# Kernel tuning notes

Measured on AMD Instinct MI355X. Metric: run time of the kernel, lower is better.

## Reference

```python
import jax, jax.numpy as jnp
import numpy as np

B, S, L = 8, 2048, 8
H, NH = 768, 12
DH = H // NH
NUM_REL = 100
LN_EPS = 1e-5


def setup_inputs() -> dict:
    key = jax.random.key(0)
    ks = jax.random.split(key, 16)
    inp = {
        'text_embeddings': jax.random.normal(ks[0], (B, S, H), dtype=jnp.float32),
        # values in [-1, 64); -1 marks 'no leaf' and is masked out
        'graph_structure': jax.random.randint(ks[1], (B, S, L), -1, 64, dtype=jnp.int64),
        'relation_ids': jax.random.randint(ks[2], (B, S, L), 0, NUM_REL, dtype=jnp.int64),
        'rel_table': jax.random.normal(ks[3], (NUM_REL, H), dtype=jnp.float32),
        'Wq': jax.random.normal(ks[4], (H, H), dtype=jnp.float32) / np.sqrt(H),
        'bq': jnp.zeros((H,), dtype=jnp.float32),
        'Wk': jax.random.normal(ks[5], (H, H), dtype=jnp.float32) / np.sqrt(H),
        'bk': jnp.zeros((H,), dtype=jnp.float32),
        'Wv': jax.random.normal(ks[6], (H, H), dtype=jnp.float32) / np.sqrt(H),
        'bv': jnp.zeros((H,), dtype=jnp.float32),
        'Wo': jax.random.normal(ks[7], (H, H), dtype=jnp.float32) / np.sqrt(H),
        'bo': jnp.zeros((H,), dtype=jnp.float32),
        'gamma': jnp.ones((H,), dtype=jnp.float32),
        'beta': jnp.zeros((H,), dtype=jnp.float32),
    }
    return inp


def reference(text_embeddings, graph_structure, relation_ids, rel_table,
              Wq, bq, Wk, bk, Wv, bv, Wo, bo, gamma, beta):
    b, s, h = text_embeddings.shape
    l = relation_ids.shape[2]
    # embedding gather (clamp -1 -> 0, masked later)
    rel_emb = rel_table[jnp.clip(relation_ids, 0, None)]  # [B,S,L,H]
    # projections; query has length-1 per root token
    q = (text_embeddings @ Wq + bq).reshape(b, s, NH, DH)          # [B,S,N,D]
    k = (rel_emb @ Wk + bk).reshape(b, s, l, NH, DH)               # [B,S,L,N,D]
    v = (rel_emb @ Wv + bv).reshape(b, s, l, NH, DH)
    scores = jnp.einsum('bsnd,bslnd->bsnl', q, k) / np.sqrt(DH)    # [B,S,N,L]
    mask = (graph_structure != -1)[:, :, None, :]                  # [B,S,1,L]
    scores = jnp.where(mask, scores, jnp.float32(-10000.0))
    probs = jax.nn.softmax(scores, axis=-1)                        # [B,S,N,L]
    ctx = jnp.einsum('bsnl,bslnd->bsnd', probs, v).reshape(b, s, h)
    out = ctx @ Wo + bo
    x = text_embeddings + out
    mu = jnp.mean(x, axis=-1, keepdims=True)
    var = jnp.mean(jnp.square(x - mu), axis=-1, keepdims=True)
    return (x - mu) * jax.lax.rsqrt(var + LN_EPS) * gamma + beta
```

## Files before the change

kernel.cpp:

```cpp
#include <hip/hip_runtime.h>
#include <hip/hip_bf16.h>

#define H 768
#define NH 12
#define DH 64
#define LL 8
#define NTOK 16384
#define NREL 100
#define NRELP 128
#define PADW 72

typedef __attribute__((ext_vector_type(8))) short short8;
typedef __attribute__((ext_vector_type(4))) float f32x4;

__device__ __forceinline__ float bf2f(ushort u) {
  union { unsigned int i; float f; } v; v.i = ((unsigned int)u) << 16; return v.f;
}
__device__ __forceinline__ float bflo(unsigned int u) {
  union { unsigned int i; float f; } v; v.i = u << 16; return v.f;
}
__device__ __forceinline__ float bfhi(unsigned int u) {
  union { unsigned int i; float f; } v; v.i = u & 0xffff0000u; return v.f;
}
__device__ __forceinline__ ushort f2bf(float f) {
  union { float f; unsigned int i; } v; v.f = f;
  unsigned int x = v.i;
  return (ushort)((x + 0x7fffu + ((x >> 16) & 1u)) >> 16);
}
__device__ __forceinline__ unsigned int cvt_pk_bf16(float lo, float hi) {
  unsigned int r;
  asm("v_cvt_pk_bf16_f32 %0, %1, %2" : "=v"(r) : "v"(lo), "v"(hi));
  return r;
}

__global__ __launch_bounds__(256) void prep_kernel(
    const float* __restrict__ s0, ushort* __restrict__ d0,
    const float* __restrict__ s1, ushort* __restrict__ d1,
    const float* __restrict__ s2, ushort* __restrict__ d2,
    const float* __restrict__ s3, ushort* __restrict__ d3,
    const float* __restrict__ rel, ushort* __restrict__ RelB) {
  if (blockIdx.z == 4) {
    int b = blockIdx.y * 24 + blockIdx.x;
    if (b < 96) {
      int i = (b * 256 + threadIdx.x) * 4;
      int row = i / H;
      ushort4 o = {0, 0, 0, 0};
      if (row < NREL) {
        float4 v = *(const float4*)(rel + i);
        o.x = f2bf(v.x); o.y = f2bf(v.y); o.z = f2bf(v.z); o.w = f2bf(v.w);
      }
      *(ushort4*)(RelB + i) = o;
    }
    return;
  }
  const float* src; ushort* dst;
  switch (blockIdx.z) {
    case 0:  src = s0; dst = d0; break;
    case 1:  src = s1; dst = d1; break;
    case 2:  src = s2; dst = d2; break;
    default: src = s3; dst = d3; break;
  }
  __shared__ float tile[32][33];
  int bx = blockIdx.x * 32, by = blockIdx.y * 32;
  int tx = threadIdx.x & 31, ty = threadIdx.x >> 5;
  #pragma unroll
  for (int i = 0; i < 32; i += 8)
    tile[ty + i][tx] = src[(size_t)(by + ty + i) * H + bx + tx];
  __syncthreads();
  #pragma unroll
  for (int i = 0; i < 32; i += 8)
    dst[(size_t)(bx + ty + i) * H + by + tx] = f2bf(tile[tx][ty + i]);
}

__device__ __forceinline__ void gload_lds16(const void* g, void* l) {
  __builtin_amdgcn_global_load_lds(
      (const __attribute__((address_space(1))) unsigned int*)g,
      (__attribute__((address_space(3))) unsigned int*)l, 16, 0, 0);
}

#define BM 128
#define BN 256
#define BK 64
#define ATILE (BM * BK)
#define BTILE (BN * BK)

#define GEMM_COMPUTE()                                                         \
  _Pragma("unroll")                                                            \
  for (int kk = 0; kk < 2; ++kk) {                                             \
    const int sw = (((kk << 2) | lk) ^ (lr & 7)) * 8;                          \
    short8 af[4], bfr[8];                                                      \
    _Pragma("unroll")                                                          \
    for (int m = 0; m < 4; ++m)                                                \
      af[m] = *(const short8*)(As + (wr * 64 + m * 16 + lr) * BK + sw);        \
    _Pragma("unroll")                                                          \
    for (int n = 0; n < 8; ++n)                                                \
      bfr[n] = *(const short8*)(Bs + (wc * 128 + n * 16 + lr) * BK + sw);      \
    _Pragma("unroll")                                                          \
    for (int m = 0; m < 4; ++m)                                                \
      _Pragma("unroll")                                                        \
      for (int n = 0; n < 8; ++n)                                              \
        acc[m][n] = __builtin_amdgcn_mfma_f32_16x16x32_bf16(af[m], bfr[n],     \
                                                            acc[m][n], 0, 0, 0);\
  }

#define GEMM_EPILOGUE()                                                        \
  _Pragma("unroll")                                                            \
  for (int m = 0; m < 4; ++m) {                                                \
    _Pragma("unroll")                                                          \
    for (int n = 0; n < 8; ++n) {                                              \
      int col = col0 + wc * 128 + n * 16 + lr;                                 \
      float b = bias[col];                                                     \
      _Pragma("unroll")                                                        \
      for (int j = 0; j < 4; ++j) {                                            \
        int row = row0 + wr * 64 + m * 16 + lk * 4 + j;                        \
        C[(size_t)row * N + col] = f2bf(acc[m][n][j] + b);                     \
      }                                                                        \
    }                                                                          \
  }

__device__ __forceinline__ void gemm_body(
    ushort* As, ushort* Bs,
    const ushort* __restrict__ A,
    const ushort* __restrict__ Bt,
    const float* __restrict__ bias,
    ushort* __restrict__ C,
    int M, int N, int K, int bx, int by) {
  const int tid = threadIdx.x;
  const int row0 = by * BM;
  const int col0 = bx * BN;
  const int wave = tid >> 6;
  const int lane = tid & 63;
  const int wr = wave >> 1, wc = wave & 1;
  const int lr = lane & 15, lk = lane >> 4;
  f32x4 acc[4][8];
  #pragma unroll
  for (int m = 0; m < 4; ++m)
    #pragma unroll
    for (int n = 0; n < 8; ++n) acc[m][n] = (f32x4)(0.f);

  for (int k0 = 0; k0 < K; k0 += BK) {
    #pragma unroll
    for (int i = 0; i < 4; ++i) {
      int c = tid + i * 256; int r = c >> 3, s = c & 7; int gsx = s ^ (r & 7);
      gload_lds16(A + (size_t)(row0 + r) * K + k0 + gsx * 8, (char*)As + c * 16);
    }
    #pragma unroll
    for (int i = 0; i < 8; ++i) {
      int c = tid + i * 256; int r = c >> 3, s = c & 7; int gsx = s ^ (r & 7);
      gload_lds16(Bt + (size_t)(col0 + r) * K + k0 + gsx * 8, (char*)Bs + c * 16);
    }
    __syncthreads();
    GEMM_COMPUTE()
    __syncthreads();
  }
  GEMM_EPILOGUE()
}

__device__ __forceinline__ void gemm_body_a32(
    ushort* As, ushort* Bs,
    const float* __restrict__ A32,
    const ushort* __restrict__ Bt,
    const float* __restrict__ bias,
    ushort* __restrict__ C,
    int M, int N, int K, int bx, int by) {
  const int tid = threadIdx.x;
  const int row0 = by * BM;
  const int col0 = bx * BN;
  const int wave = tid >> 6;
  const int lane = tid & 63;
  const int wr = wave >> 1, wc = wave & 1;
  const int lr = lane & 15, lk = lane >> 4;
  f32x4 acc[4][8];
  #pragma unroll
  for (int m = 0; m < 4; ++m)
    #pragma unroll
    for (int n = 0; n < 8; ++n) acc[m][n] = (f32x4)(0.f);

  for (int k0 = 0; k0 < K; k0 += BK) {
    #pragma unroll
    for (int i = 0; i < 8; ++i) {
      int c = tid + i * 256; int r = c >> 3, s = c & 7; int gsx = s ^ (r & 7);
      gload_lds16(Bt + (size_t)(col0 + r) * K + k0 + gsx * 8, (char*)Bs + c * 16);
    }
    #pragma unroll
    for (int i = 0; i < 4; ++i) {
      int c = tid + i * 256; int r = c >> 3, s = c & 7; int gsx = s ^ (r & 7);
      const float* src = A32 + (size_t)(row0 + r) * K + k0 + gsx * 8;
      float4 f0 = *(const float4*)(src);
      float4 f1 = *(const float4*)(src + 4);
      uint4 w;
      w.x = cvt_pk_bf16(f0.x, f0.y);
      w.y = cvt_pk_bf16(f0.z, f0.w);
      w.z = cvt_pk_bf16(f1.x, f1.y);
      w.w = cvt_pk_bf16(f1.z, f1.w);
      *(uint4*)((char*)As + c * 16) = w;
    }
    __syncthreads();
    GEMM_COMPUTE()
    __syncthreads();
  }
  GEMM_EPILOGUE()
}

__global__ __launch_bounds__(256, 2) void gemm_q_kv_kernel(
    const float* __restrict__ X, const ushort* __restrict__ WqT,
    const float* __restrict__ bq, ushort* __restrict__ Qbf,
    const ushort* __restrict__ RelB,
    const ushort* __restrict__ WkT, const float* __restrict__ bk, ushort* __restrict__ Ktab,
    const ushort* __restrict__ WvT, const float* __restrict__ bv, ushort* __restrict__ Vtab) {
  __shared__ ushort As[ATILE];
  __shared__ ushort Bs[BTILE];
  int lin = blockIdx.x;
  if (lin < 6) {
    if (lin < 3)
      gemm_body(As, Bs, RelB, WkT, bk, Ktab, NRELP, H, H, lin, 0);
    else
      gemm_body(As, Bs, RelB, WvT, bv, Vtab, NRELP, H, H, lin - 3, 0);
    return;
  }
  int l2 = lin - 6;
  int wg = (l2 & 7) * 48 + (l2 >> 3);
  gemm_body_a32(As, Bs, X, WqT, bq, Qbf, NTOK, H, H, wg % 3, wg / 3);
}

__global__ __launch_bounds__(256, 2) void gemm_bt_kernel(
    const ushort* __restrict__ A, const ushort* __restrict__ Bt,
    const float* __restrict__ bias, ushort* __restrict__ C,
    int M, int N, int K) {
  __shared__ ushort As[ATILE];
  __shared__ ushort Bs[BTILE];
  int lin = blockIdx.y * gridDim.x + blockIdx.x;
  int q = (gridDim.x * gridDim.y) >> 3;
  int wg = (lin & 7) * q + (lin >> 3);
  gemm_body(As, Bs, A, Bt, bias, C, M, N, K, wg % gridDim.x, wg / gridDim.x);
}

__global__ __launch_bounds__(256) void attn3_kernel(
    const ushort* __restrict__ Q,
    const ushort* __restrict__ Ktab,
    const ushort* __restrict__ Vtab,
    const int* __restrict__ graph,
    const int* __restrict__ relid,
    ushort* __restrict__ Ctx) {
  __shared__ __align__(16) ushort Ks[NREL * PADW];
  __shared__ __align__(16) ushort Vs[NREL * PADW];
  const int tid = threadIdx.x;
  const int head = blockIdx.y;
  const int t = blockIdx.x * 256 + tid;

  #pragma unroll
  for (int i = 0; i < 4; ++i) {
    int c = tid + i * 256;
    if (c < NREL * 9) {
      int row = c / 9, slot = c - row * 9;
      int gsx = (slot < 8) ? slot * 8 : 0;
      const size_t src = (size_t)row * H + head * DH + gsx;
      gload_lds16(Ktab + src, (char*)Ks + (size_t)c * 16);
      gload_lds16(Vtab + src, (char*)Vs + (size_t)c * 16);
    }
  }

  const uint4* qp = (const uint4*)(Q + (size_t)t * H + head * DH);
  uint4 qw[8];
  #pragma unroll
  for (int j = 0; j < 8; ++j) qw[j] = qp[j];
  const int4* gp = (const int4*)(graph + (size_t)t * LL);
  const int4* rp = (const int4*)(relid + (size_t)t * LL);
  int4 ga = gp[0], gb = gp[1];
  int4 ra = rp[0], rb = rp[1];
  int gs[8] = {ga.x, ga.y, ga.z, ga.w, gb.x, gb.y, gb.z, gb.w};
  int rid[8] = {ra.x, ra.y, ra.z, ra.w, rb.x, rb.y, rb.z, rb.w};
  int koff[8];
  #pragma unroll
  for (int l = 0; l < 8; ++l) {
    int r = rid[l] < 0 ? 0 : rid[l];
    koff[l] = r * (PADW * 2);
  }

  __syncthreads();

  float s[8];
  #pragma unroll
  for (int l = 0; l < 8; ++l) s[l] = 0.f;
  #pragma unroll
  for (int j = 0; j < 8; ++j) {
    float qf[8];
    qf[0] = bflo(qw[j].x); qf[1] = bfhi(qw[j].x);
    qf[2] = bflo(qw[j].y); qf[3] = bfhi(qw[j].y);
    qf[4] = bflo(qw[j].z); qf[5] = bfhi(qw[j].z);
    qf[6] = bflo(qw[j].w); qf[7] = bfhi(qw[j].w);
    #pragma unroll
    for (int l = 0; l < 8; ++l) {
      uint4 kw = *(const uint4*)((const char*)Ks + koff[l] + j * 16);
      s[l] += qf[0] * bflo(kw.x) + qf[1] * bfhi(kw.x)
            + qf[2] * bflo(kw.y) + qf[3] * bfhi(kw.y)
            + qf[4] * bflo(kw.z) + qf[5] * bfhi(kw.z)
            + qf[6] * bflo(kw.w) + qf[7] * bfhi(kw.w);
    }
  }

  #pragma unroll
  for (int l = 0; l < 8; ++l)
    s[l] = (gs[l] != -1) ? s[l] * 0.125f : -10000.0f;
  float mx = s[0];
  #pragma unroll
  for (int l = 1; l < 8; ++l) mx = fmaxf(mx, s[l]);
  float p[8], den = 0.f;
  #pragma unroll
  for (int l = 0; l < 8; ++l) { p[l] = __expf(s[l] - mx); den += p[l]; }
  float inv = 1.f / den;
  #pragma unroll
  for (int l = 0; l < 8; ++l) p[l] *= inv;

  ushort* cp = Ctx + (size_t)t * H + head * DH;
  #pragma unroll
  for (int j = 0; j < 8; ++j) {
    float a[8];
    #pragma unroll
    for (int d = 0; d < 8; ++d) a[d] = 0.f;
    #pragma unroll
    for (int l = 0; l < 8; ++l) {
      uint4 vw = *(const uint4*)((const char*)Vs + koff[l] + j * 16);
      a[0] += p[l] * bflo(vw.x); a[1] += p[l] * bfhi(vw.x);
      a[2] += p[l] * bflo(vw.y); a[3] += p[l] * bfhi(vw.y);
      a[4] += p[l] * bflo(vw.z); a[5] += p[l] * bfhi(vw.z);
      a[6] += p[l] * bflo(vw.w); a[7] += p[l] * bfhi(vw.w);
    }
    short8 o;
    #pragma unroll
    for (int d = 0; d < 8; ++d) o[d] = (short)f2bf(a[d]);
    *(short8*)(cp + j * 8) = o;
  }
}

__global__ __launch_bounds__(192) void ln_kernel(
    const float* __restrict__ text, const ushort* __restrict__ op,
    const float* __restrict__ gamma, const float* __restrict__ beta,
    float* __restrict__ out) {
  int t = blockIdx.x;
  int c0 = threadIdx.x * 4;
  float4 tv = *(const float4*)(text + (size_t)t * H + c0);
  ushort4 ov = *(const ushort4*)(op + (size_t)t * H + c0);
  float x0 = tv.x + bf2f(ov.x), x1 = tv.y + bf2f(ov.y);
  float x2 = tv.z + bf2f(ov.z), x3 = tv.w + bf2f(ov.w);
  float s = x0 + x1 + x2 + x3;
  float s2 = x0 * x0 + x1 * x1 + x2 * x2 + x3 * x3;
  #pragma unroll
  for (int off = 32; off > 0; off >>= 1) {
    s  += __shfl_xor(s, off, 64);
    s2 += __shfl_xor(s2, off, 64);
  }
  __shared__ float red[2][3];
  int wave = threadIdx.x >> 6, lane = threadIdx.x & 63;
  if (lane == 0) { red[0][wave] = s; red[1][wave] = s2; }
  __syncthreads();
  s  = red[0][0] + red[0][1] + red[0][2];
  s2 = red[1][0] + red[1][1] + red[1][2];
  float mu = s * (1.f / H);
  float var = s2 * (1.f / H) - mu * mu;
  float rs = rsqrtf(var + 1e-5f);
  float4 g4 = *(const float4*)(gamma + c0);
  float4 b4 = *(const float4*)(beta + c0);
  float4 o4;
  o4.x = (x0 - mu) * rs * g4.x + b4.x;
  o4.y = (x1 - mu) * rs * g4.y + b4.y;
  o4.z = (x2 - mu) * rs * g4.z + b4.z;
  o4.w = (x3 - mu) * rs * g4.w + b4.w;
  *(float4*)(out + (size_t)t * H + c0) = o4;
}

extern "C" void kernel_launch(void* const* d_in, const int* in_sizes, int n_in,
                              void* d_out, int out_size, void* d_ws, size_t ws_size,
                              hipStream_t stream) {
  const float* text      = (const float*)d_in[0];
  const int*   graph     = (const int*)d_in[1];
  const int*   relid     = (const int*)d_in[2];
  const float* rel_table = (const float*)d_in[3];
  const float* Wq = (const float*)d_in[4];  const float* bq = (const float*)d_in[5];
  const float* Wk = (const float*)d_in[6];  const float* bk = (const float*)d_in[7];
  const float* Wv = (const float*)d_in[8];  const float* bv = (const float*)d_in[9];
  const float* Wo = (const float*)d_in[10]; const float* bo = (const float*)d_in[11];
  const float* gamma = (const float*)d_in[12];
  const float* beta  = (const float*)d_in[13];
  float* out = (float*)d_out;
  char* ws = (char*)d_ws;

  const size_t TOKH = (size_t)NTOK * H;
  size_t off = 0;
  ushort* Ctx  = (ushort*)(ws + off); off += TOKH * 2;
  ushort* Qbf  = (ushort*)(ws + off); off += TOKH * 2;
  ushort* WqT  = (ushort*)(ws + off); off += (size_t)H * H * 2;
  ushort* WoT  = (ushort*)(ws + off); off += (size_t)H * H * 2;
  ushort* WkT  = (ushort*)(ws + off); off += (size_t)H * H * 2;
  ushort* WvT  = (ushort*)(ws + off); off += (size_t)H * H * 2;
  ushort* RelB = (ushort*)(ws + off); off += (size_t)NRELP * H * 2;
  ushort* Ktab = (ushort*)(ws + off); off += (size_t)NRELP * H * 2;
  ushort* Vtab = (ushort*)(ws + off); off += (size_t)NRELP * H * 2;

  prep_kernel<<<dim3(24, 24, 5), 256, 0, stream>>>(
      Wq, WqT, Wo, WoT, Wk, WkT, Wv, WvT, rel_table, RelB);
  gemm_q_kv_kernel<<<6 + 384, 256, 0, stream>>>(
      text, WqT, bq, Qbf, RelB, WkT, bk, Ktab, WvT, bv, Vtab);
  dim3 ga(NTOK / 256, NH);
  attn3_kernel<<<ga, 256, 0, stream>>>(Qbf, Ktab, Vtab, graph, relid, Ctx);
  dim3 g1(H / BN, NTOK / BM);
  gemm_bt_kernel<<<g1, 256, 0, stream>>>(Ctx, WoT, bo, Qbf, NTOK, H, H);
  ln_kernel<<<NTOK, 192, 0, stream>>>(text, Qbf, gamma, beta, out);
}
```

Before: 101.8 us.

## Double-buffer GEMM LDS tiles with async global-to-LDS loads and 8 waves

Rewrites both GEMM bodies as a two-stage pipeline. The tile for step t+2 is staged into the alternate LDS buffer with global_load_lds while the current buffer is consumed, and the loop uses explicit vmcnt waits and barriers. Workgroups grow to 512 threads (8 waves, 4x4 MFMA tiles per wave). The fp32 activation A tile for the Q projection is now copied straight into LDS and converted to bf16 when fragments are read, which removes the register round-trip in the global load path. The goal is to hide global-load latency behind MFMA work, at the cost of much larger LDS use (up to 128KB per block), which lowers block occupancy.

Measured after the change: 118.5 us. 16.4% more time.

```diff
diff --git a/kernel.cpp b/kernel.cpp
--- a/kernel.cpp
+++ b/kernel.cpp
@@ -81,34 +81,32 @@
 #define BM 128
 #define BN 256
 #define BK 64
-#define ATILE (BM * BK)
-#define BTILE (BN * BK)
-
-#define GEMM_COMPUTE()                                                         \
-  _Pragma("unroll")                                                            \
-  for (int kk = 0; kk < 2; ++kk) {                                             \
-    const int sw = (((kk << 2) | lk) ^ (lr & 7)) * 8;                          \
-    short8 af[4], bfr[8];                                                      \
-    _Pragma("unroll")                                                          \
-    for (int m = 0; m < 4; ++m)                                                \
-      af[m] = *(const short8*)(As + (wr * 64 + m * 16 + lr) * BK + sw);        \
-    _Pragma("unroll")                                                          \
-    for (int n = 0; n < 8; ++n)                                                \
-      bfr[n] = *(const short8*)(Bs + (wc * 128 + n * 16 + lr) * BK + sw);      \
-    _Pragma("unroll")                                                          \
-    for (int m = 0; m < 4; ++m)                                                \
-      _Pragma("unroll")                                                        \
-      for (int n = 0; n < 8; ++n)                                              \
-        acc[m][n] = __builtin_amdgcn_mfma_f32_16x16x32_bf16(af[m], bfr[n],     \
-                                                            acc[m][n], 0, 0, 0);\
-  }
-
-#define GEMM_EPILOGUE()                                                        \
+
+#define SBAR()   __builtin_amdgcn_s_barrier()
+#define SCHED0() __builtin_amdgcn_sched_barrier(0)
+
+#define STG_A16(k0, cbuf)                                                      \
+  _Pragma("unroll") for (int i = 0; i < 2; ++i) {                              \
+    int c = tid + i * 512; int r = c >> 3, s = c & 7; int g = s ^ (r & 7);     \
+    gload_lds16(A + (size_t)(row0 + r) * K + (k0) + g * 8,                     \
+                Ab + (cbuf) * 16384 + c * 16); }
+#define STG_A32(k0, cbuf)                                                      \
+  _Pragma("unroll") for (int i = 0; i < 4; ++i) {                              \
+    int c = tid + i * 512; int r = c >> 4, s = c & 15; int g = s ^ (r & 15);   \
+    gload_lds16(A32 + (size_t)(row0 + r) * K + (k0) + g * 4,                   \
+                Ab + (cbuf) * 32768 + c * 16); }
+#define STG_B(k0, cbuf)                                                        \
+  _Pragma("unroll") for (int i = 0; i < 4; ++i) {                              \
+    int c = tid + i * 512; int r = c >> 3, s = c & 7; int g = s ^ (r & 7);     \
+    gload_lds16(Bt + (size_t)(col0 + r) * K + (k0) + g * 8,                    \
+                Bb + (cbuf) * 32768 + c * 16); }
+
+#define PIPE_EPILOGUE()                                                        \
   _Pragma("unroll")                                                            \
   for (int m = 0; m < 4; ++m) {                                                \
     _Pragma("unroll")                                                          \
-    for (int n = 0; n < 8; ++n) {                                              \
-      int col = col0 + wc * 128 + n * 16 + lr;                                 \
+    for (int n = 0; n < 4; ++n) {                                              \
+      int col = col0 + wc * 64 + n * 16 + lr;                                  \
       float b = bias[col];                                                     \
       _Pragma("unroll")                                                        \
       for (int j = 0; j < 4; ++j) {                                            \
@@ -118,121 +116,154 @@
     }                                                                          \
   }
 
-__device__ __forceinline__ void gemm_body(
-    ushort* As, ushort* Bs,
-    const ushort* __restrict__ A,
-    const ushort* __restrict__ Bt,
-    const float* __restrict__ bias,
-    ushort* __restrict__ C,
+__device__ __forceinline__ void gemm_pipe_bf16(
+    char* Ab, char* Bb,
+    const ushort* __restrict__ A, const ushort* __restrict__ Bt,
+    const float* __restrict__ bias, ushort* __restrict__ C,
     int M, int N, int K, int bx, int by) {
   const int tid = threadIdx.x;
-  const int row0 = by * BM;
-  const int col0 = bx * BN;
-  const int wave = tid >> 6;
-  const int lane = tid & 63;
-  const int wr = wave >> 1, wc = wave & 1;
+  const int row0 = by * BM, col0 = bx * BN;
+  const int wave = tid >> 6, lane = tid & 63;
+  const int wr = wave >> 2, wc = wave & 3;
   const int lr = lane & 15, lk = lane >> 4;
-  f32x4 acc[4][8];
+  f32x4 acc[4][4];
   #pragma unroll
   for (int m = 0; m < 4; ++m)
     #pragma unroll
-    for (int n = 0; n < 8; ++n) acc[m][n] = (f32x4)(0.f);
-
-  for (int k0 = 0; k0 < K; k0 += BK) {
-    #pragma unroll
-    for (int i = 0; i < 4; ++i) {
-      int c = tid + i * 256; int r = c >> 3, s = c & 7; int gsx = s ^ (r & 7);
-      gload_lds16(A + (size_t)(row0 + r) * K + k0 + gsx * 8, (char*)As + c * 16);
-    }
-    #pragma unroll
-    for (int i = 0; i < 8; ++i) {
-      int c = tid + i * 256; int r = c >> 3, s = c & 7; int gsx = s ^ (r & 7);
-      gload_lds16(Bt + (size_t)(col0 + r) * K + k0 + gsx * 8, (char*)Bs + c * 16);
-    }
-    __syncthreads();
-    GEMM_COMPUTE()
-    __syncthreads();
-  }
-  GEMM_EPILOGUE()
-}
-
-__device__ __forceinline__ void gemm_body_a32(
-    ushort* As, ushort* Bs,
-    const float* __restrict__ A32,
-    const ushort* __restrict__ Bt,
-    const float* __restrict__ bias,
-    ushort* __restrict__ C,
+    for (int n = 0; n < 4; ++n) acc[m][n] = (f32x4)(0.f);
+  const int nt = K / BK;
+
+  STG_A16(0, 0) STG_B(0, 0)
+  STG_A16(BK, 1) STG_B(BK, 1)
+  asm volatile("s_waitcnt vmcnt(6)" ::: "memory");
+  SCHED0(); SBAR();
+  int cb = 0;
+  for (int t = 0; t < nt; ++t) {
+    #pragma unroll
+    for (int kk = 0; kk < 2; ++kk) {
+      const int sw = (((kk << 2) | lk) ^ (lr & 7)) * 16;
+      short8 af[4], bfr[4];
+      #pragma unroll
+      for (int m = 0; m < 4; ++m)
+        af[m] = *(const short8*)(Ab + cb * 16384 + (wr * 64 + m * 16 + lr) * 128 + sw);
+      #pragma unroll
+      for (int n = 0; n < 4; ++n)
+        bfr[n] = *(const short8*)(Bb + cb * 32768 + (wc * 64 + n * 16 + lr) * 128 + sw);
+      #pragma unroll
+      for (int m = 0; m < 4; ++m)
+        #pragma unroll
+        for (int n = 0; n < 4; ++n)
+          acc[m][n] = __builtin_amdgcn_mfma_f32_16x16x32_bf16(af[m], bfr[n], acc[m][n], 0, 0, 0);
+    }
+    if (t == nt - 1) break;
+    SBAR(); SCHED0();
+    if (t + 2 < nt) {
+      STG_A16((t + 2) * BK, cb) STG_B((t + 2) * BK, cb)
+      asm volatile("s_waitcnt vmcnt(6)" ::: "memory");
+    } else {
+      asm volatile("s_waitcnt vmcnt(0)" ::: "memory");
+    }
+    SCHED0(); SBAR();
+    cb ^= 1;
+  }
+  PIPE_EPILOGUE()
+}
+
+__device__ __forceinline__ void gemm_pipe_a32(
+    char* Ab, char* Bb,
+    const float* __restrict__ A32, const ushort* __restrict__ Bt,
+    const float* __restrict__ bias, ushort* __restrict__ C,
     int M, int N, int K, int bx, int by) {
   const int tid = threadIdx.x;
-  const int row0 = by * BM;
-  const int col0 = bx * BN;
-  const int wave = tid >> 6;
-  const int lane = tid & 63;
-  const int wr = wave >> 1, wc = wave & 1;
+  const int row0 = by * BM, col0 = bx * BN;
+  const int wave = tid >> 6, lane = tid & 63;
+  const int wr = wave >> 2, wc = wave & 3;
   const int lr = lane & 15, lk = lane >> 4;
-  f32x4 acc[4][8];
+  f32x4 acc[4][4];
   #pragma unroll
   for (int m = 0; m < 4; ++m)
     #pragma unroll
-    for (int n = 0; n < 8; ++n) acc[m][n] = (f32x4)(0.f);
-
-  for (int k0 = 0; k0 < K; k0 += BK) {
-    #pragma unroll
-    for (int i = 0; i < 8; ++i) {
-      int c = tid + i * 256; int r = c >> 3, s = c & 7; int gsx = s ^ (r & 7);
-      gload_lds16(Bt + (size_t)(col0 + r) * K + k0 + gsx * 8, (char*)Bs + c * 16);
-    }
-    #pragma unroll
-    for (int i = 0; i < 4; ++i) {
-      int c = tid + i * 256; int r = c >> 3, s = c & 7; int gsx = s ^ (r & 7);
-      const float* src = A32 + (size_t)(row0 + r) * K + k0 + gsx * 8;
-      float4 f0 = *(const float4*)(src);
-      float4 f1 = *(const float4*)(src + 4);
-      uint4 w;
-      w.x = cvt_pk_bf16(f0.x, f0.y);
-      w.y = cvt_pk_bf16(f0.z, f0.w);
-      w.z = cvt_pk_bf16(f1.x, f1.y);
-      w.w = cvt_pk_bf16(f1.z, f1.w);
-      *(uint4*)((char*)As + c * 16) = w;
-    }
-    __syncthreads();
-    GEMM_COMPUTE()
-    __syncthreads();
-  }
-  GEMM_EPILOGUE()
-}
-
-__global__ __launch_bounds__(256, 2) void gemm_q_kv_kernel(
+    for (int n = 0; n < 4; ++n) acc[m][n] = (f32x4)(0.f);
+  const int nt = K / BK;
+
+  STG_A32(0, 0) STG_B(0, 0)
+  STG_A32(BK, 1) STG_B(BK, 1)
+  asm volatile("s_waitcnt vmcnt(8)" ::: "memory");
+  SCHED0(); SBAR();
+  int cb = 0;
+  for (int t = 0; t < nt; ++t) {
+    #pragma unroll
+    for (int kk = 0; kk < 2; ++kk) {
+      const int sw = (((kk << 2) | lk) ^ (lr & 7)) * 16;
+      short8 af[4], bfr[4];
+      #pragma unroll
+      for (int m = 0; m < 4; ++m) {
+        const int R = wr * 64 + m * 16 + lr;
+        const int c0 = (kk << 3) + (lk << 1);
+        const char* base = Ab + cb * 32768 + R * 256;
+        union { uint4 u; float4 f; } fa, fb;
+        fa.u = *(const uint4*)(base + ((c0 ^ lr) * 16));
+        fb.u = *(const uint4*)(base + (((c0 + 1) ^ lr) * 16));
+        union { uint4 u; short8 s8; } w;
+        w.u.x = cvt_pk_bf16(fa.f.x, fa.f.y);
+        w.u.y = cvt_pk_bf16(fa.f.z, fa.f.w);
+        w.u.z = cvt_pk_bf16(fb.f.x, fb.f.y);
+        w.u.w = cvt_pk_bf16(fb.f.z, fb.f.w);
+        af[m] = w.s8;
+      }
+      #pragma unroll
+      for (int n = 0; n < 4; ++n)
+        bfr[n] = *(const short8*)(Bb + cb * 32768 + (wc * 64 + n * 16 + lr) * 128 + sw);
+      #pragma unroll
+      for (int m = 0; m < 4; ++m)
+        #pragma unroll
+        for (int n = 0; n < 4; ++n)
+          acc[m][n] = __builtin_amdgcn_mfma_f32_16x16x32_bf16(af[m], bfr[n], acc[m][n], 0, 0, 0);
+    }
+    if (t == nt - 1) break;
+    SBAR(); SCHED0();
+    if (t + 2 < nt) {
+      STG_A32((t + 2) * BK, cb) STG_B((t + 2) * BK, cb)
+      asm volatile("s_waitcnt vmcnt(8)" ::: "memory");
+    } else {
+      asm volatile("s_waitcnt vmcnt(0)" ::: "memory");
+    }
+    SCHED0(); SBAR();
+    cb ^= 1;
+  }
+  PIPE_EPILOGUE()
+}
+
+__global__ __launch_bounds__(512, 2) void gemm_q_kv_kernel(
     const float* __restrict__ X, const ushort* __restrict__ WqT,
     const float* __restrict__ bq, ushort* __restrict__ Qbf,
     const ushort* __restrict__ RelB,
     const ushort* __restrict__ WkT, const float* __restrict__ bk, ushort* __restrict__ Ktab,
     const ushort* __restrict__ WvT, const float* __restrict__ bv, ushort* __restrict__ Vtab) {
-  __shared__ ushort As[ATILE];
-  __shared__ ushort Bs[BTILE];
+  __shared__ char lds[131072];
   int lin = blockIdx.x;
   if (lin < 6) {
     if (lin < 3)
-      gemm_body(As, Bs, RelB, WkT, bk, Ktab, NRELP, H, H, lin, 0);
+      gemm_pipe_bf16(lds, lds + 65536, RelB, WkT, bk, Ktab, NRELP, H, H, lin, 0);
     else
-      gemm_body(As, Bs, RelB, WvT, bv, Vtab, NRELP, H, H, lin - 3, 0);
+      gemm_pipe_bf16(lds, lds + 65536, RelB, WvT, bv, Vtab, NRELP, H, H, lin - 3, 0);
     return;
   }
   int l2 = lin - 6;
   int wg = (l2 & 7) * 48 + (l2 >> 3);
-  gemm_body_a32(As, Bs, X, WqT, bq, Qbf, NTOK, H, H, wg % 3, wg / 3);
-}
-
-__global__ __launch_bounds__(256, 2) void gemm_bt_kernel(
+  gemm_pipe_a32(lds, lds + 65536, X, WqT, bq, Qbf, NTOK, H, H, wg % 3, wg / 3);
+}
+
+__global__ __launch_bounds__(512, 2) void gemm_bt_kernel(
     const ushort* __restrict__ A, const ushort* __restrict__ Bt,
     const float* __restrict__ bias, ushort* __restrict__ C,
     int M, int N, int K) {
-  __shared__ ushort As[ATILE];
-  __shared__ ushort Bs[BTILE];
+  __shared__ char lds[98304];
   int lin = blockIdx.y * gridDim.x + blockIdx.x;
   int q = (gridDim.x * gridDim.y) >> 3;
   int wg = (lin & 7) * q + (lin >> 3);
-  gemm_body(As, Bs, A, Bt, bias, C, M, N, K, wg % gridDim.x, wg / gridDim.x);
+  gemm_pipe_bf16(lds, lds + 32768, A, Bt, bias, C, M, N, K,
+                 wg % gridDim.x, wg / gridDim.x);
 }
 
 __global__ __launch_bounds__(256) void attn3_kernel(
@@ -399,11 +430,11 @@
 
   prep_kernel<<<dim3(24, 24, 5), 256, 0, stream>>>(
       Wq, WqT, Wo, WoT, Wk, WkT, Wv, WvT, rel_table, RelB);
-  gemm_q_kv_kernel<<<6 + 384, 256, 0, stream>>>(
+  gemm_q_kv_kernel<<<6 + 384, 512, 0, stream>>>(
       text, WqT, bq, Qbf, RelB, WkT, bk, Ktab, WvT, bv, Vtab);
   dim3 ga(NTOK / 256, NH);
   attn3_kernel<<<ga, 256, 0, stream>>>(Qbf, Ktab, Vtab, graph, relid, Ctx);
   dim3 g1(H / BN, NTOK / BM);
-  gemm_bt_kernel<<<g1, 256, 0, stream>>>(Ctx, WoT, bo, Qbf, NTOK, H, H);
+  gemm_bt_kernel<<<g1, 512, 0, stream>>>(Ctx, WoT, bo, Qbf, NTOK, H, H);
   ln_kernel<<<NTOK, 192, 0, stream>>>(text, Qbf, gamma, beta, out);
 }
```

## Fuse Q projection, attention and output projection into one persistent mega kernel

Applied to the files above, without the earlier changes.

Replaces the separate Q GEMM, attention and output GEMM launches with a single kernel. Each 512-thread block handles 64 tokens: it stages the full X row-block in LDS as bf16, computes Q into LDS per 256-column chunk, runs attention for four heads straight from that LDS Q, then restages Ctx and runs the Wo GEMM. The K/V table GEMMs move to a small separate 12-block kernel. This removes the Q round trip through global memory and two launches. In exchange, only 256 blocks run at one block per CU, attention reads K/V from global/L2 instead of LDS, and half the threads sit idle during attention.

After: 197.4 us. 93.9% more time.

```diff
diff --git a/kernel.cpp b/kernel.cpp
--- a/kernel.cpp
+++ b/kernel.cpp
@@ -8,7 +8,6 @@
 #define NTOK 16384
 #define NREL 100
 #define NRELP 128
-#define PADW 72
 
 typedef __attribute__((ext_vector_type(8))) short short8;
 typedef __attribute__((ext_vector_type(4))) float f32x4;
@@ -78,258 +77,242 @@
       (__attribute__((address_space(3))) unsigned int*)l, 16, 0, 0);
 }
 
-#define BM 128
-#define BN 256
-#define BK 64
-#define ATILE (BM * BK)
-#define BTILE (BN * BK)
-
-#define GEMM_COMPUTE()                                                         \
+__device__ __forceinline__ void stage_A_bf16(char* Xs, const ushort* A, int row0) {
+  const int tid = threadIdx.x;
+  #pragma unroll
+  for (int i = 0; i < 12; ++i) {
+    int c = tid + i * 512;
+    int r = c / 96, p = c - r * 96;
+    gload_lds16(A + (size_t)(row0 + r) * H + ((p ^ (r & 7)) << 3), Xs + (size_t)c * 16);
+  }
+}
+
+__device__ __forceinline__ void stage_A_f32cvt(char* Xs, const float* X, int row0) {
+  const int tid = threadIdx.x;
+  #pragma unroll
+  for (int i = 0; i < 12; ++i) {
+    int c = tid + i * 512;
+    int r = c / 96, p = c - r * 96;
+    const float* src = X + (size_t)(row0 + r) * H + p * 8;
+    float4 f0 = *(const float4*)src;
+    float4 f1 = *(const float4*)(src + 4);
+    uint4 w;
+    w.x = cvt_pk_bf16(f0.x, f0.y); w.y = cvt_pk_bf16(f0.z, f0.w);
+    w.z = cvt_pk_bf16(f1.x, f1.y); w.w = cvt_pk_bf16(f1.z, f1.w);
+    *(uint4*)(Xs + r * 1536 + ((p ^ (r & 7)) * 16)) = w;
+  }
+}
+
+#define CHUNK_GEMM(BT, colbase)                                                \
+  for (int t = 0; t < 12; ++t) {                                               \
+    const int k0 = t * 64;                                                     \
+    _Pragma("unroll")                                                          \
+    for (int i = 0; i < 4; ++i) {                                              \
+      int c = tid + i * 512; int rr = c >> 3, ss = c & 7; int g = ss ^ (rr & 7); \
+      gload_lds16((BT) + (size_t)((colbase) + rr) * H + k0 + g * 8,            \
+                  Bst + (size_t)c * 16);                                       \
+    }                                                                          \
+    __syncthreads();                                                           \
+    _Pragma("unroll")                                                          \
+    for (int kk = 0; kk < 2; ++kk) {                                           \
+      short8 af[2], bfr[4];                                                    \
+      _Pragma("unroll")                                                        \
+      for (int m = 0; m < 2; ++m) {                                            \
+        int row = wr * 32 + m * 16 + lr;                                       \
+        int ch = (k0 >> 3) + (kk << 2) + lk;                                   \
+        af[m] = *(const short8*)(Xs + row * 1536 + ((ch ^ (row & 7)) * 16));   \
+      }                                                                        \
+      const int sw = (((kk << 2) | lk) ^ (lr & 7)) * 16;                       \
+      _Pragma("unroll")                                                        \
+      for (int nn = 0; nn < 4; ++nn)                                           \
+        bfr[nn] = *(const short8*)(Bst + (wc * 64 + nn * 16 + lr) * 128 + sw); \
+      _Pragma("unroll")                                                        \
+      for (int m = 0; m < 2; ++m)                                              \
+        _Pragma("unroll")                                                      \
+        for (int nn = 0; nn < 4; ++nn)                                         \
+          acc[m][nn] = __builtin_amdgcn_mfma_f32_16x16x32_bf16(               \
+              af[m], bfr[nn], acc[m][nn], 0, 0, 0);                            \
+    }                                                                          \
+    __syncthreads();                                                           \
+  }
+
+#define CHUNK_EPI_GLOBAL(COUT, BIAS, colbase, row0)                            \
   _Pragma("unroll")                                                            \
-  for (int kk = 0; kk < 2; ++kk) {                                             \
-    const int sw = (((kk << 2) | lk) ^ (lr & 7)) * 8;                          \
-    short8 af[4], bfr[8];                                                      \
+  for (int m = 0; m < 2; ++m)                                                  \
     _Pragma("unroll")                                                          \
-    for (int m = 0; m < 4; ++m)                                                \
-      af[m] = *(const short8*)(As + (wr * 64 + m * 16 + lr) * BK + sw);        \
-    _Pragma("unroll")                                                          \
-    for (int n = 0; n < 8; ++n)                                                \
-      bfr[n] = *(const short8*)(Bs + (wc * 128 + n * 16 + lr) * BK + sw);      \
-    _Pragma("unroll")                                                          \
-    for (int m = 0; m < 4; ++m)                                                \
-      _Pragma("unroll")                                                        \
-      for (int n = 0; n < 8; ++n)                                              \
-        acc[m][n] = __builtin_amdgcn_mfma_f32_16x16x32_bf16(af[m], bfr[n],     \
-                                                            acc[m][n], 0, 0, 0);\
-  }
-
-#define GEMM_EPILOGUE()                                                        \
-  _Pragma("unroll")                                                            \
-  for (int m = 0; m < 4; ++m) {                                                \
-    _Pragma("unroll")                                                          \
-    for (int n = 0; n < 8; ++n) {                                              \
-      int col = col0 + wc * 128 + n * 16 + lr;                                 \
-      float b = bias[col];                                                     \
+    for (int nn = 0; nn < 4; ++nn) {                                           \
+      int col = (colbase) + wc * 64 + nn * 16 + lr;                            \
+      float b = (BIAS)[col];                                                   \
       _Pragma("unroll")                                                        \
       for (int j = 0; j < 4; ++j) {                                            \
-        int row = row0 + wr * 64 + m * 16 + lk * 4 + j;                        \
-        C[(size_t)row * N + col] = f2bf(acc[m][n][j] + b);                     \
+        int row = (row0) + wr * 32 + m * 16 + lk * 4 + j;                      \
+        (COUT)[(size_t)row * H + col] = f2bf(acc[m][nn][j] + b);               \
       }                                                                        \
-    }                                                                          \
-  }
-
-__device__ __forceinline__ void gemm_body(
-    ushort* As, ushort* Bs,
-    const ushort* __restrict__ A,
-    const ushort* __restrict__ Bt,
-    const float* __restrict__ bias,
-    ushort* __restrict__ C,
-    int M, int N, int K, int bx, int by) {
-  const int tid = threadIdx.x;
-  const int row0 = by * BM;
-  const int col0 = bx * BN;
-  const int wave = tid >> 6;
-  const int lane = tid & 63;
-  const int wr = wave >> 1, wc = wave & 1;
-  const int lr = lane & 15, lk = lane >> 4;
-  f32x4 acc[4][8];
-  #pragma unroll
-  for (int m = 0; m < 4; ++m)
-    #pragma unroll
-    for (int n = 0; n < 8; ++n) acc[m][n] = (f32x4)(0.f);
-
-  for (int k0 = 0; k0 < K; k0 += BK) {
-    #pragma unroll
-    for (int i = 0; i < 4; ++i) {
-      int c = tid + i * 256; int r = c >> 3, s = c & 7; int gsx = s ^ (r & 7);
-      gload_lds16(A + (size_t)(row0 + r) * K + k0 + gsx * 8, (char*)As + c * 16);
-    }
-    #pragma unroll
-    for (int i = 0; i < 8; ++i) {
-      int c = tid + i * 256; int r = c >> 3, s = c & 7; int gsx = s ^ (r & 7);
-      gload_lds16(Bt + (size_t)(col0 + r) * K + k0 + gsx * 8, (char*)Bs + c * 16);
-    }
-    __syncthreads();
-    GEMM_COMPUTE()
-    __syncthreads();
-  }
-  GEMM_EPILOGUE()
-}
-
-__device__ __forceinline__ void gemm_body_a32(
-    ushort* As, ushort* Bs,
-    const float* __restrict__ A32,
-    const ushort* __restrict__ Bt,
-    const float* __restrict__ bias,
-    ushort* __restrict__ C,
-    int M, int N, int K, int bx, int by) {
-  const int tid = threadIdx.x;
-  const int row0 = by * BM;
-  const int col0 = bx * BN;
-  const int wave = tid >> 6;
-  const int lane = tid & 63;
-  const int wr = wave >> 1, wc = wave & 1;
-  const int lr = lane & 15, lk = lane >> 4;
-  f32x4 acc[4][8];
-  #pragma unroll
-  for (int m = 0; m < 4; ++m)
-    #pragma unroll
-    for (int n = 0; n < 8; ++n) acc[m][n] = (f32x4)(0.f);
-
-  for (int k0 = 0; k0 < K; k0 += BK) {
-    #pragma unroll
-    for (int i = 0; i < 8; ++i) {
-      int c = tid + i * 256; int r = c >> 3, s = c & 7; int gsx = s ^ (r & 7);
-      gload_lds16(Bt + (size_t)(col0 + r) * K + k0 + gsx * 8, (char*)Bs + c * 16);
-    }
-    #pragma unroll
-    for (int i = 0; i < 4; ++i) {
-      int c = tid + i * 256; int r = c >> 3, s = c & 7; int gsx = s ^ (r & 7);
-      const float* src = A32 + (size_t)(row0 + r) * K + k0 + gsx * 8;
-      float4 f0 = *(const float4*)(src);
-      float4 f1 = *(const float4*)(src + 4);
-      uint4 w;
-      w.x = cvt_pk_bf16(f0.x, f0.y);
-      w.y = cvt_pk_bf16(f0.z, f0.w);
-      w.z = cvt_pk_bf16(f1.x, f1.y);
-      w.w = cvt_pk_bf16(f1.z, f1.w);
-      *(uint4*)((char*)As + c * 16) = w;
-    }
-    __syncthreads();
-    GEMM_COMPUTE()
-    __syncthreads();
-  }
-  GEMM_EPILOGUE()
-}
-
-__global__ __launch_bounds__(256, 2) void gemm_q_kv_kernel(
-    const float* __restrict__ X, const ushort* __restrict__ WqT,
-    const float* __restrict__ bq, ushort* __restrict__ Qbf,
+    }
+
+__global__ __launch_bounds__(512, 1) void kv12_kernel(
     const ushort* __restrict__ RelB,
     const ushort* __restrict__ WkT, const float* __restrict__ bk, ushort* __restrict__ Ktab,
     const ushort* __restrict__ WvT, const float* __restrict__ bv, ushort* __restrict__ Vtab) {
-  __shared__ ushort As[ATILE];
-  __shared__ ushort Bs[BTILE];
-  int lin = blockIdx.x;
-  if (lin < 6) {
-    if (lin < 3)
-      gemm_body(As, Bs, RelB, WkT, bk, Ktab, NRELP, H, H, lin, 0);
-    else
-      gemm_body(As, Bs, RelB, WvT, bv, Vtab, NRELP, H, H, lin - 3, 0);
-    return;
-  }
-  int l2 = lin - 6;
-  int wg = (l2 & 7) * 48 + (l2 >> 3);
-  gemm_body_a32(As, Bs, X, WqT, bq, Qbf, NTOK, H, H, wg % 3, wg / 3);
-}
-
-__global__ __launch_bounds__(256, 2) void gemm_bt_kernel(
-    const ushort* __restrict__ A, const ushort* __restrict__ Bt,
-    const float* __restrict__ bias, ushort* __restrict__ C,
-    int M, int N, int K) {
-  __shared__ ushort As[ATILE];
-  __shared__ ushort Bs[BTILE];
-  int lin = blockIdx.y * gridDim.x + blockIdx.x;
-  int q = (gridDim.x * gridDim.y) >> 3;
-  int wg = (lin & 7) * q + (lin >> 3);
-  gemm_body(As, Bs, A, Bt, bias, C, M, N, K, wg % gridDim.x, wg / gridDim.x);
-}
-
-__global__ __launch_bounds__(256) void attn3_kernel(
-    const ushort* __restrict__ Q,
-    const ushort* __restrict__ Ktab,
-    const ushort* __restrict__ Vtab,
-    const int* __restrict__ graph,
-    const int* __restrict__ relid,
-    ushort* __restrict__ Ctx) {
-  __shared__ __align__(16) ushort Ks[NREL * PADW];
-  __shared__ __align__(16) ushort Vs[NREL * PADW];
+  __shared__ char lds[131072];
+  char* Xs = lds;
+  char* Bst = lds + 98304;
   const int tid = threadIdx.x;
-  const int head = blockIdx.y;
-  const int t = blockIdx.x * 256 + tid;
-
-  #pragma unroll
-  for (int i = 0; i < 4; ++i) {
-    int c = tid + i * 256;
-    if (c < NREL * 9) {
-      int row = c / 9, slot = c - row * 9;
-      int gsx = (slot < 8) ? slot * 8 : 0;
-      const size_t src = (size_t)row * H + head * DH + gsx;
-      gload_lds16(Ktab + src, (char*)Ks + (size_t)c * 16);
-      gload_lds16(Vtab + src, (char*)Vs + (size_t)c * 16);
-    }
-  }
-
-  const uint4* qp = (const uint4*)(Q + (size_t)t * H + head * DH);
-  uint4 qw[8];
-  #pragma unroll
-  for (int j = 0; j < 8; ++j) qw[j] = qp[j];
-  const int4* gp = (const int4*)(graph + (size_t)t * LL);
-  const int4* rp = (const int4*)(relid + (size_t)t * LL);
-  int4 ga = gp[0], gb = gp[1];
-  int4 ra = rp[0], rb = rp[1];
-  int gs[8] = {ga.x, ga.y, ga.z, ga.w, gb.x, gb.y, gb.z, gb.w};
-  int rid[8] = {ra.x, ra.y, ra.z, ra.w, rb.x, rb.y, rb.z, rb.w};
-  int koff[8];
-  #pragma unroll
-  for (int l = 0; l < 8; ++l) {
-    int r = rid[l] < 0 ? 0 : rid[l];
-    koff[l] = r * (PADW * 2);
-  }
-
-  __syncthreads();
-
-  float s[8];
-  #pragma unroll
-  for (int l = 0; l < 8; ++l) s[l] = 0.f;
-  #pragma unroll
-  for (int j = 0; j < 8; ++j) {
-    float qf[8];
-    qf[0] = bflo(qw[j].x); qf[1] = bfhi(qw[j].x);
-    qf[2] = bflo(qw[j].y); qf[3] = bfhi(qw[j].y);
-    qf[4] = bflo(qw[j].z); qf[5] = bfhi(qw[j].z);
-    qf[6] = bflo(qw[j].w); qf[7] = bfhi(qw[j].w);
+  const int wave = tid >> 6, lane = tid & 63;
+  const int wr = wave >> 2, wc = wave & 3;
+  const int lr = lane & 15, lk = lane >> 4;
+  int bb = blockIdx.x;
+  const ushort* Bt; const float* bias; ushort* Cout;
+  if (bb < 6) { Bt = WkT; bias = bk; Cout = Ktab; }
+  else        { Bt = WvT; bias = bv; Cout = Vtab; bb -= 6; }
+  const int mb = bb / 3, nb = bb % 3;
+  const int row0 = mb * 64;
+  stage_A_bf16(Xs, RelB, row0);
+  __syncthreads();
+  {
+    f32x4 acc[2][4];
     #pragma unroll
-    for (int l = 0; l < 8; ++l) {
-      uint4 kw = *(const uint4*)((const char*)Ks + koff[l] + j * 16);
-      s[l] += qf[0] * bflo(kw.x) + qf[1] * bfhi(kw.x)
-            + qf[2] * bflo(kw.y) + qf[3] * bfhi(kw.y)
-            + qf[4] * bflo(kw.z) + qf[5] * bfhi(kw.z)
-            + qf[6] * bflo(kw.w) + qf[7] * bfhi(kw.w);
-    }
-  }
-
-  #pragma unroll
-  for (int l = 0; l < 8; ++l)
-    s[l] = (gs[l] != -1) ? s[l] * 0.125f : -10000.0f;
-  float mx = s[0];
-  #pragma unroll
-  for (int l = 1; l < 8; ++l) mx = fmaxf(mx, s[l]);
-  float p[8], den = 0.f;
-  #pragma unroll
-  for (int l = 0; l < 8; ++l) { p[l] = __expf(s[l] - mx); den += p[l]; }
-  float inv = 1.f / den;
-  #pragma unroll
-  for (int l = 0; l < 8; ++l) p[l] *= inv;
-
-  ushort* cp = Ctx + (size_t)t * H + head * DH;
-  #pragma unroll
-  for (int j = 0; j < 8; ++j) {
-    float a[8];
-    #pragma unroll
-    for (int d = 0; d < 8; ++d) a[d] = 0.f;
-    #pragma unroll
-    for (int l = 0; l < 8; ++l) {
-      uint4 vw = *(const uint4*)((const char*)Vs + koff[l] + j * 16);
-      a[0] += p[l] * bflo(vw.x); a[1] += p[l] * bfhi(vw.x);
-      a[2] += p[l] * bflo(vw.y); a[3] += p[l] * bfhi(vw.y);
-      a[4] += p[l] * bflo(vw.z); a[5] += p[l] * bfhi(vw.z);
-      a[6] += p[l] * bflo(vw.w); a[7] += p[l] * bfhi(vw.w);
-    }
-    short8 o;
-    #pragma unroll
-    for (int d = 0; d < 8; ++d) o[d] = (short)f2bf(a[d]);
-    *(short8*)(cp + j * 8) = o;
+    for (int m = 0; m < 2; ++m)
+      #pragma unroll
+      for (int nn = 0; nn < 4; ++nn) acc[m][nn] = (f32x4)(0.f);
+    CHUNK_GEMM(Bt, nb * 256)
+    CHUNK_EPI_GLOBAL(Cout, bias, nb * 256, row0)
+  }
+}
+
+__global__ __launch_bounds__(512, 1) void mega_kernel(
+    const float* __restrict__ X,
+    const ushort* __restrict__ WqT, const float* __restrict__ bq,
+    const ushort* __restrict__ WoT, const float* __restrict__ bo,
+    const ushort* __restrict__ Ktab, const ushort* __restrict__ Vtab,
+    const int* __restrict__ graph, const int* __restrict__ relid,
+    ushort* __restrict__ Ctx, ushort* __restrict__ OP) {
+  __shared__ char lds[131072];
+  char* Xs = lds;
+  char* Bst = lds + 98304;
+  const int tid = threadIdx.x;
+  const int blk = blockIdx.x;
+  const int wg = (blk & 7) * 32 + (blk >> 3);
+  const int tok0 = wg * 64;
+  const int wave = tid >> 6, lane = tid & 63;
+  const int wr = wave >> 2, wc = wave & 3;
+  const int lr = lane & 15, lk = lane >> 4;
+
+  stage_A_f32cvt(Xs, X, tok0);
+  __syncthreads();
+
+  for (int n = 0; n < 3; ++n) {
+    const int col0 = n * 256;
+    {
+      f32x4 acc[2][4];
+      #pragma unroll
+      for (int m = 0; m < 2; ++m)
+        #pragma unroll
+        for (int nn = 0; nn < 4; ++nn) acc[m][nn] = (f32x4)(0.f);
+      CHUNK_GEMM(WqT, col0)
+      #pragma unroll
+      for (int m = 0; m < 2; ++m)
+        #pragma unroll
+        for (int nn = 0; nn < 4; ++nn) {
+          int colc = wc * 64 + nn * 16 + lr;
+          float b = bq[col0 + colc];
+          int cpos = colc >> 3;
+          #pragma unroll
+          for (int j = 0; j < 4; ++j) {
+            int row = wr * 32 + m * 16 + lk * 4 + j;
+            *(ushort*)(Bst + row * 512 + ((cpos ^ (row & 7)) * 16) + (colc & 7) * 2)
+                = f2bf(acc[m][nn][j] + b);
+          }
+        }
+    }
+    __syncthreads();
+    if (tid < 256) {
+      const int t = tid >> 2, hh = tid & 3;
+      const int h = n * 4 + hh;
+      const int gtok = tok0 + t;
+      uint4 qw[8];
+      #pragma unroll
+      for (int k = 0; k < 8; ++k)
+        qw[k] = *(const uint4*)(Bst + t * 512 + ((((hh << 3) + k) ^ (t & 7)) * 16));
+      const int4* gp = (const int4*)(graph + (size_t)gtok * LL);
+      const int4* rp = (const int4*)(relid + (size_t)gtok * LL);
+      int4 ga = gp[0], gb = gp[1];
+      int4 ra = rp[0], rb = rp[1];
+      int gs[8] = {ga.x, ga.y, ga.z, ga.w, gb.x, gb.y, gb.z, gb.w};
+      int rid[8] = {ra.x, ra.y, ra.z, ra.w, rb.x, rb.y, rb.z, rb.w};
+      size_t koff[8];
+      #pragma unroll
+      for (int l = 0; l < 8; ++l) {
+        int r = rid[l] < 0 ? 0 : rid[l];
+        koff[l] = (size_t)r * H + h * DH;
+      }
+      float s[8];
+      #pragma unroll
+      for (int l = 0; l < 8; ++l) s[l] = 0.f;
+      #pragma unroll
+      for (int j = 0; j < 8; ++j) {
+        float qf[8];
+        qf[0] = bflo(qw[j].x); qf[1] = bfhi(qw[j].x);
+        qf[2] = bflo(qw[j].y); qf[3] = bfhi(qw[j].y);
+        qf[4] = bflo(qw[j].z); qf[5] = bfhi(qw[j].z);
+        qf[6] = bflo(qw[j].w); qf[7] = bfhi(qw[j].w);
+        #pragma unroll
+        for (int l = 0; l < 8; ++l) {
+          uint4 kw = *(const uint4*)(Ktab + koff[l] + j * 8);
+          s[l] += qf[0] * bflo(kw.x) + qf[1] * bfhi(kw.x)
+                + qf[2] * bflo(kw.y) + qf[3] * bfhi(kw.y)
+                + qf[4] * bflo(kw.z) + qf[5] * bfhi(kw.z)
+                + qf[6] * bflo(kw.w) + qf[7] * bfhi(kw.w);
+        }
+      }
+      #pragma unroll
+      for (int l = 0; l < 8; ++l)
+        s[l] = (gs[l] != -1) ? s[l] * 0.125f : -10000.0f;
+      float mx = s[0];
+      #pragma unroll
+      for (int l = 1; l < 8; ++l) mx = fmaxf(mx, s[l]);
+      float p[8], den = 0.f;
+      #pragma unroll
+      for (int l = 0; l < 8; ++l) { p[l] = __expf(s[l] - mx); den += p[l]; }
+      float inv = 1.f / den;
+      #pragma unroll
+      for (int l = 0; l < 8; ++l) p[l] *= inv;
+      ushort* cp = Ctx + (size_t)gtok * H + h * DH;
+      #pragma unroll
+      for (int j = 0; j < 8; ++j) {
+        float a[8];
+        #pragma unroll
+        for (int d = 0; d < 8; ++d) a[d] = 0.f;
+        #pragma unroll
+        for (int l = 0; l < 8; ++l) {
+          uint4 vw = *(const uint4*)(Vtab + koff[l] + j * 8);
+          a[0] += p[l] * bflo(vw.x); a[1] += p[l] * bfhi(vw.x);
+          a[2] += p[l] * bflo(vw.y); a[3] += p[l] * bfhi(vw.y);
+          a[4] += p[l] * bflo(vw.z); a[5] += p[l] * bfhi(vw.z);
+          a[6] += p[l] * bflo(vw.w); a[7] += p[l] * bfhi(vw.w);
+        }
+        short8 o;
+        #pragma unroll
+        for (int d = 0; d < 8; ++d) o[d] = (short)f2bf(a[d]);
+        *(short8*)(cp + j * 8) = o;
+      }
+    }
+    __syncthreads();
+  }
+
+  stage_A_bf16(Xs, Ctx, tok0);
+  __syncthreads();
+  for (int n = 0; n < 3; ++n) {
+    const int col0 = n * 256;
+    {
+      f32x4 acc[2][4];
+      #pragma unroll
+      for (int m = 0; m < 2; ++m)
+        #pragma unroll
+        for (int nn = 0; nn < 4; ++nn) acc[m][nn] = (f32x4)(0.f);
+      CHUNK_GEMM(WoT, col0)
+      CHUNK_EPI_GLOBAL(OP, bo, col0, tok0)
+    }
   }
 }
 
@@ -399,11 +382,8 @@
 
   prep_kernel<<<dim3(24, 24, 5), 256, 0, stream>>>(
       Wq, WqT, Wo, WoT, Wk, WkT, Wv, WvT, rel_table, RelB);
-  gemm_q_kv_kernel<<<6 + 384, 256, 0, stream>>>(
-      text, WqT, bq, Qbf, RelB, WkT, bk, Ktab, WvT, bv, Vtab);
-  dim3 ga(NTOK / 256, NH);
-  attn3_kernel<<<ga, 256, 0, stream>>>(Qbf, Ktab, Vtab, graph, relid, Ctx);
-  dim3 g1(H / BN, NTOK / BM);
-  gemm_bt_kernel<<<g1, 256, 0, stream>>>(Ctx, WoT, bo, Qbf, NTOK, H, H);
+  kv12_kernel<<<12, 512, 0, stream>>>(RelB, WkT, bk, Ktab, WvT, bv, Vtab);
+  mega_kernel<<<256, 512, 0, stream>>>(
+      text, WqT, bq, WoT, bo, Ktab, Vtab, graph, relid, Ctx, Qbf);
   ln_kernel<<<NTOK, 192, 0, stream>>>(text, Qbf, gamma, beta, out);
 }
```
